# Optimization experiments

Measured on AMD Instinct MI355X. Metric: run time of the kernel, lower is better.

Reference implementation:

```python
import jax, jax.numpy as jnp
import numpy as np

H = 1024   # GRU hidden size
Z = 1024   # latent z dim
A = 4      # action dim
F = 30     # number of expert MLPs / max horizon
DIN = Z + H      # 2048, expert MLP input
DH = 512         # expert MLP hidden
EIN = H + 94     # evalMLP input (belief + pos/ori one-hot)
EH = 512
EOUT = 94


def setup_inputs() -> dict:
    key = jax.random.key(0)
    ks = jax.random.split(key, 20)
    s = 0.02
    inp = {
        "b_t": jax.random.normal(ks[0], (1, H), jnp.float32),
        "a_t": jax.random.normal(ks[1], (F, A), jnp.float32),
        "z_tp1_pos": jax.random.normal(ks[2], (F, Z), jnp.float32),
        "z_tp1_neg": jax.random.normal(ks[3], (F, Z), jnp.float32),
        "init_pos_ori": jax.random.uniform(ks[4], (1, 94), jnp.float32),
        # action GRU params (PyTorch layout: W_ih (3H, A), W_hh (3H, H))
        "gru_Wih": jax.random.normal(ks[5], (3 * H, A), jnp.float32) * s,
        "gru_Whh": jax.random.normal(ks[6], (3 * H, H), jnp.float32) * s,
        "gru_bih": jax.random.normal(ks[7], (3 * H,), jnp.float32) * s,
        "gru_bhh": jax.random.normal(ks[8], (3 * H,), jnp.float32) * s,
        # 30 stacked expert MLPs: Linear(DIN,DH)+ReLU+Linear(DH,1)
        "mlp_W1": jax.random.normal(ks[9], (F, DIN, DH), jnp.float32) * s,
        "mlp_b1": jax.random.normal(ks[10], (F, DH), jnp.float32) * s,
        "mlp_W2": jax.random.normal(ks[11], (F, DH, 1), jnp.float32) * s,
        "mlp_b2": jax.random.normal(ks[12], (F, 1), jnp.float32) * s,
        # evalMLP: Linear(EIN,EH)+ReLU+Linear(EH,EOUT)+sigmoid
        "eval_W1": jax.random.normal(ks[13], (EIN, EH), jnp.float32) * s,
        "eval_b1": jax.random.normal(ks[14], (EH,), jnp.float32) * s,
        "eval_W2": jax.random.normal(ks[15], (EH, EOUT), jnp.float32) * s,
        "eval_b2": jax.random.normal(ks[16], (EOUT,), jnp.float32) * s,
        "f": F,
    }
    return inp


def _gru(x, h0, Wih, Whh, bih, bhh):
    # x: (T, A), h0: (H,) -> outputs (T, H). PyTorch nn.GRU cell math.
    def step(h, xt):
        gi = Wih @ xt + bih          # (3H,)
        gh = Whh @ h + bhh           # (3H,)
        ir, iz, inn = jnp.split(gi, 3)
        hr, hz, hn = jnp.split(gh, 3)
        r = jax.nn.sigmoid(ir + hr)
        z = jax.nn.sigmoid(iz + hz)
        n = jnp.tanh(inn + r * hn)
        h_new = (1.0 - z) * n + z * h
        return h_new, h_new
    _, hs = jax.lax.scan(step, h0, x)
    return hs


def _experts(x, W1, b1, W2, b2, f):
    # x: (f, DIN); expert i applied to row i only (grouped batch-1 GEMMs).
    h = jax.nn.relu(jnp.einsum('fi,fih->fh', x, W1[:f]) + b1[:f])
    return jnp.einsum('fh,fho->fo', h, W2[:f]) + b2[:f]   # (f, 1) logits


def reference(b_t, a_t, z_tp1_pos, z_tp1_neg, init_pos_ori,
              gru_Wih, gru_Whh, gru_bih, gru_bhh,
              mlp_W1, mlp_b1, mlp_W2, mlp_b2,
              eval_W1, eval_b1, eval_W2, eval_b2, f):
    a_gru = _gru(a_t[:f], b_t[0], gru_Wih, gru_Whh, gru_bih, gru_bhh)  # (f, H)
    z_pos = jnp.concatenate([z_tp1_pos[:f], a_gru], axis=1)           # (f, Z+H)
    pred_positive = _experts(z_pos, mlp_W1, mlp_b1, mlp_W2, mlp_b2, f)
    z_neg = jnp.concatenate([z_tp1_neg[:f], a_gru], axis=1)
    pred_negative = _experts(z_neg, mlp_W1, mlp_b1, mlp_W2, mlp_b2, f)
    # eval branch uses b_t.detach()
    eval_in = jnp.concatenate([jax.lax.stop_gradient(b_t), init_pos_ori], axis=1)
    eh = jax.nn.relu(eval_in @ eval_W1 + eval_b1)
    pred_xytheta = jax.nn.sigmoid(eh @ eval_W2 + eval_b2)             # (1, 94)
    return pred_positive, pred_negative, pred_xytheta
```

## Files before the change

kernel.cpp:

```cpp
#include <hip/hip_runtime.h>
#include <math.h>

constexpr int kH    = 1024;
constexpr int kZ    = 1024;
constexpr int kA    = 4;
constexpr int kF    = 30;
constexpr int kDIN  = 2048;
constexpr int kDH   = 512;
constexpr int kEIN  = 1118;
constexpr int kEH   = 512;
constexpr int kEOUT = 94;

constexpr int GRU_NB  = 64;
constexpr int EXP_PRT = 8;

constexpr size_t HACC_OFF = 0;
constexpr size_t EHA_OFF  = HACC_OFF + (size_t)kF * 2 * EXP_PRT * kDH;
constexpr size_t TAG_OFF  = EHA_OFF + (size_t)8 * kEH;

__device__ __forceinline__ float sigmoidf_(float x) { return 1.0f / (1.0f + __expf(-x)); }

__device__ __forceinline__ float wave_reduce(float v) {
#pragma unroll
  for (int off = 32; off > 0; off >>= 1) v += __shfl_down(v, off, 64);
  return v;
}

__device__ __forceinline__ unsigned long long tag_ld(const unsigned long long* p) {
  return __hip_atomic_load(p, __ATOMIC_RELAXED, __HIP_MEMORY_SCOPE_AGENT);
}

__device__ __forceinline__ void tag_pub(unsigned long long* p, unsigned long long v) {
  (void)__hip_atomic_exchange(p, v, __ATOMIC_RELAXED, __HIP_MEMORY_SCOPE_AGENT);
}

__global__ __launch_bounds__(512) void gru64(const float* __restrict__ Whh,
                                             const float* __restrict__ bhh,
                                             const float* __restrict__ Wih,
                                             const float* __restrict__ bih,
                                             const float* __restrict__ a_t,
                                             const float* __restrict__ b_t,
                                             unsigned long long* __restrict__ tagbuf,
                                             const int* __restrict__ fptr) {
  const int bid  = blockIdx.x;
  const int tid  = threadIdx.x;
  const int wave = tid >> 6;
  const int lane = tid & 63;
  const int f    = *fptr;

  const int jb = bid * 16;
  const int j0 = jb + wave;
  const int j1 = jb + wave + 8;

  __shared__ float gis[kF][16][3];
  __shared__ __align__(16) float hs[kH];

  const float4* W4 = (const float4*)Whh;
  float4 wr0[4], wz0[4], wn0[4], wr1[4], wz1[4], wn1[4];
#pragma unroll
  for (int i = 0; i < 4; i++) {
    wr0[i] = W4[(size_t)j0 * 256 + i * 64 + lane];
    wz0[i] = W4[(size_t)(j0 + kH) * 256 + i * 64 + lane];
    wn0[i] = W4[(size_t)(j0 + 2 * kH) * 256 + i * 64 + lane];
    wr1[i] = W4[(size_t)j1 * 256 + i * 64 + lane];
    wz1[i] = W4[(size_t)(j1 + kH) * 256 + i * 64 + lane];
    wn1[i] = W4[(size_t)(j1 + 2 * kH) * 256 + i * 64 + lane];
  }
  const float b0r = bhh[j0], b0z = bhh[j0 + kH], b0n = bhh[j0 + 2 * kH];
  const float b1r = bhh[j1], b1z = bhh[j1 + kH], b1n = bhh[j1 + 2 * kH];

  for (int idx = tid; idx < kF * 16 * 3; idx += 512) {
    int t = idx / 48;
    int rem = idx - t * 48;
    int w = rem / 3, g = rem - w * 3;
    int r = jb + w + g * kH;
    float acc = bih[r];
    const float* wih = Wih + (size_t)r * kA;
    const float* at  = a_t + (size_t)t * kA;
#pragma unroll
    for (int k = 0; k < kA; k++) acc += wih[k] * at[k];
    gis[t][w][g] = acc;
  }
  __syncthreads();

  const float4* hs4 = (const float4*)hs;
  for (int t = 0; t < f; t++) {
    if (t == 0) {
      hs[tid]       = b_t[tid];
      hs[tid + 512] = b_t[tid + 512];
    } else {
      const unsigned long long* tg = tagbuf + (size_t)(t - 1) * kH;
      const unsigned want = (unsigned)t;
      unsigned long long v0 = tag_ld(tg + tid);
      unsigned long long v1 = tag_ld(tg + tid + 512);
      while ((unsigned)(v0 >> 32) != want) v0 = tag_ld(tg + tid);
      while ((unsigned)(v1 >> 32) != want) v1 = tag_ld(tg + tid + 512);
      hs[tid]       = __uint_as_float((unsigned)v0);
      hs[tid + 512] = __uint_as_float((unsigned)v1);
    }
    __syncthreads();

    float a0r = 0.f, a0z = 0.f, a0n = 0.f, a1r = 0.f, a1z = 0.f, a1n = 0.f;
#pragma unroll
    for (int i = 0; i < 4; i++) {
      float4 h4 = hs4[i * 64 + lane];
      a0r += wr0[i].x * h4.x + wr0[i].y * h4.y + wr0[i].z * h4.z + wr0[i].w * h4.w;
      a0z += wz0[i].x * h4.x + wz0[i].y * h4.y + wz0[i].z * h4.z + wz0[i].w * h4.w;
      a0n += wn0[i].x * h4.x + wn0[i].y * h4.y + wn0[i].z * h4.z + wn0[i].w * h4.w;
      a1r += wr1[i].x * h4.x + wr1[i].y * h4.y + wr1[i].z * h4.z + wr1[i].w * h4.w;
      a1z += wz1[i].x * h4.x + wz1[i].y * h4.y + wz1[i].z * h4.z + wz1[i].w * h4.w;
      a1n += wn1[i].x * h4.x + wn1[i].y * h4.y + wn1[i].z * h4.z + wn1[i].w * h4.w;
    }
    a0r = wave_reduce(a0r); a0z = wave_reduce(a0z); a0n = wave_reduce(a0n);
    a1r = wave_reduce(a1r); a1z = wave_reduce(a1z); a1n = wave_reduce(a1n);

    if (lane == 0) {
      float rg = sigmoidf_(gis[t][wave][0] + a0r + b0r);
      float zg = sigmoidf_(gis[t][wave][1] + a0z + b0z);
      float ng = tanhf(gis[t][wave][2] + rg * (a0n + b0n));
      float h0 = (1.0f - zg) * ng + zg * hs[j0];
      rg = sigmoidf_(gis[t][wave + 8][0] + a1r + b1r);
      zg = sigmoidf_(gis[t][wave + 8][1] + a1z + b1z);
      ng = tanhf(gis[t][wave + 8][2] + rg * (a1n + b1n));
      float h1 = (1.0f - zg) * ng + zg * hs[j1];

      const unsigned long long tg = (unsigned long long)(unsigned)(t + 1) << 32;
      tag_pub(tagbuf + (size_t)t * kH + j0, tg | (unsigned long long)__float_as_uint(h0));
      tag_pub(tagbuf + (size_t)t * kH + j1, tg | (unsigned long long)__float_as_uint(h1));
    }
    __syncthreads();
  }
}

__global__ __launch_bounds__(512) void experts(const float* __restrict__ zpos,
                                               const float* __restrict__ zneg,
                                               const unsigned long long* __restrict__ tagbuf,
                                               const float* __restrict__ W1,
                                               const float* __restrict__ b_t,
                                               const float* __restrict__ ipo,
                                               const float* __restrict__ eW1,
                                               float* __restrict__ hacc,
                                               float* __restrict__ ehacc,
                                               const int* __restrict__ fptr) {
  const int bid = blockIdx.x;
  const int tid = threadIdx.x;
  const int f   = *fptr;

  if (bid < kF * EXP_PRT) {
    __shared__ float xs_p[256];
    __shared__ float xs_n[256];
    int e = bid >> 3, part = bid & 7;
    if (e >= f) return;

    if (part < 4) {
      int r0 = part * 256;
      if (tid < 256) {
        xs_p[tid] = zpos[(size_t)e * kZ + r0 + tid];
        xs_n[tid] = zneg[(size_t)e * kZ + r0 + tid];
      }
      __syncthreads();
      float ap = 0.f, an = 0.f;
      const float* w = W1 + ((size_t)e * kDIN + r0) * kDH + tid;
#pragma unroll 8
      for (int r = 0; r < 256; r++) {
        float wv = w[(size_t)r * kDH];
        ap += xs_p[r] * wv;
        an += xs_n[r] * wv;
      }
      hacc[(((size_t)e * 2 + 0) * EXP_PRT + part) * kDH + tid] = ap;
      hacc[(((size_t)e * 2 + 1) * EXP_PRT + part) * kDH + tid] = an;
    } else {
      int r0 = (part - 4) * 256;
      if (tid < 256)
        xs_p[tid] = __uint_as_float((unsigned)tagbuf[(size_t)e * kH + r0 + tid]);
      __syncthreads();
      float a = 0.f;
      const float* w = W1 + ((size_t)e * kDIN + kZ + r0) * kDH + tid;
#pragma unroll 8
      for (int r = 0; r < 256; r++) a += xs_p[r] * w[(size_t)r * kDH];
      hacc[(((size_t)e * 2 + 0) * EXP_PRT + part) * kDH + tid] = a;
      hacc[(((size_t)e * 2 + 1) * EXP_PRT + part) * kDH + tid] = a;
    }
  } else {
    __shared__ float evs[140];
    int part = bid - kF * EXP_PRT;
    int r0 = part * 140;
    int nr = min(140, kEIN - r0);
    if (tid < nr) {
      int r = r0 + tid;
      evs[tid] = (r < kH) ? b_t[r] : ipo[r - kH];
    }
    __syncthreads();
    float acc = 0.f;
    const float* w = eW1 + (size_t)r0 * kEH + tid;
    for (int r = 0; r < nr; r++) acc += evs[r] * w[(size_t)r * kEH];
    ehacc[(size_t)part * kEH + tid] = acc;
  }
}

__global__ __launch_bounds__(512) void stage2(const float* __restrict__ hacc,
                                              const float* __restrict__ ehacc,
                                              const float* __restrict__ b1,
                                              const float* __restrict__ W2,
                                              const float* __restrict__ b2,
                                              const float* __restrict__ eb1,
                                              const float* __restrict__ eW2,
                                              const float* __restrict__ eb2,
                                              float* __restrict__ out,
                                              const int* __restrict__ fptr) {
  int b = blockIdx.x;
  int tid = threadIdx.x;
  int f = *fptr;
  if (b < kF) {
    int i = b;
    if (i >= f) return;
    float sp = 0.f, sn = 0.f;
#pragma unroll
    for (int p = 0; p < EXP_PRT; p++) {
      sp += hacc[(((size_t)i * 2 + 0) * EXP_PRT + p) * kDH + tid];
      sn += hacc[(((size_t)i * 2 + 1) * EXP_PRT + p) * kDH + tid];
    }
    float bias = b1[(size_t)i * kDH + tid];
    float hp = fmaxf(sp + bias, 0.f);
    float hn = fmaxf(sn + bias, 0.f);
    float w = W2[(size_t)i * kDH + tid];
    float pp = wave_reduce(hp * w);
    float pn = wave_reduce(hn * w);
    __shared__ float redp[8];
    __shared__ float redn[8];
    int wave = tid >> 6, lane = tid & 63;
    if (lane == 0) { redp[wave] = pp; redn[wave] = pn; }
    __syncthreads();
    if (tid == 0) {
      float s0 = 0.f, s1 = 0.f;
#pragma unroll
      for (int k = 0; k < 8; k++) { s0 += redp[k]; s1 += redn[k]; }
      out[i] = s0 + b2[i];
      out[f + i] = s1 + b2[i];
    }
  } else {
    __shared__ float ehs[kEH];
    {
      float s = eb1[tid];
#pragma unroll
      for (int p = 0; p < 8; p++) s += ehacc[(size_t)p * kEH + tid];
      ehs[tid] = fmaxf(s, 0.f);
    }
    __syncthreads();
    if (tid < kEOUT) {
      float acc = eb2[tid];
      for (int h = 0; h < kEH; h++) acc += ehs[h] * eW2[(size_t)h * kEOUT + tid];
      out[2 * f + tid] = sigmoidf_(acc);
    }
  }
}

extern "C" void kernel_launch(void* const* d_in, const int* in_sizes, int n_in,
                              void* d_out, int out_size, void* d_ws, size_t ws_size,
                              hipStream_t stream) {
  const float* b_t  = (const float*)d_in[0];
  const float* a_t  = (const float*)d_in[1];
  const float* zpos = (const float*)d_in[2];
  const float* zneg = (const float*)d_in[3];
  const float* ipo  = (const float*)d_in[4];
  const float* gWih = (const float*)d_in[5];
  const float* gWhh = (const float*)d_in[6];
  const float* gbih = (const float*)d_in[7];
  const float* gbhh = (const float*)d_in[8];
  const float* mW1  = (const float*)d_in[9];
  const float* mb1  = (const float*)d_in[10];
  const float* mW2  = (const float*)d_in[11];
  const float* mb2  = (const float*)d_in[12];
  const float* eW1  = (const float*)d_in[13];
  const float* eb1  = (const float*)d_in[14];
  const float* eW2  = (const float*)d_in[15];
  const float* eb2  = (const float*)d_in[16];
  const int*   fptr = (const int*)d_in[17];

  float* ws     = (float*)d_ws;
  float* hacc   = ws + HACC_OFF;
  float* ehacc  = ws + EHA_OFF;
  unsigned long long* tagbuf = (unsigned long long*)(ws + TAG_OFF);
  float* out    = (float*)d_out;

  gru64<<<GRU_NB, 512, 0, stream>>>(gWhh, gbhh, gWih, gbih, a_t, b_t, tagbuf, fptr);

  experts<<<kF * EXP_PRT + 8, 512, 0, stream>>>(zpos, zneg, tagbuf, mW1, b_t, ipo, eW1,
                                                hacc, ehacc, fptr);

  stage2<<<kF + 1, 512, 0, stream>>>(hacc, ehacc, mb1, mW2, mb2, eb1, eW2, eb2, out, fptr);
}
```

Before: 351.6 us.

## Spread GRU over 128 blocks with one hidden row per wave and LDS weights

The persistent GRU kernel now uses 128 blocks of 8 rows each instead of 64 blocks of 16. Each wave computes one hidden unit, and the W_hh slices move from registers into LDS (96 KB per block). The tag publish changes from an atomic exchange to an atomic store. The aim is to halve per-wave work on the serial critical path and cut register pressure. In exchange, twice as many blocks poll the tag buffer each step, and every step reads the weights from LDS instead of registers.

Result: faster. 342.7 us (-2.5%).

```diff
diff --git a/kernel.cpp b/kernel.cpp
--- a/kernel.cpp
+++ b/kernel.cpp
@@ -11,7 +11,8 @@
 constexpr int kEH   = 512;
 constexpr int kEOUT = 94;
 
-constexpr int GRU_NB  = 64;
+constexpr int GRU_NB = 128;
+constexpr int RPB    = 8;
 constexpr int EXP_PRT = 8;
 
 constexpr size_t HACC_OFF = 0;
@@ -29,49 +30,43 @@
 __device__ __forceinline__ unsigned long long tag_ld(const unsigned long long* p) {
   return __hip_atomic_load(p, __ATOMIC_RELAXED, __HIP_MEMORY_SCOPE_AGENT);
 }
-
-__device__ __forceinline__ void tag_pub(unsigned long long* p, unsigned long long v) {
-  (void)__hip_atomic_exchange(p, v, __ATOMIC_RELAXED, __HIP_MEMORY_SCOPE_AGENT);
-}
-
-__global__ __launch_bounds__(512) void gru64(const float* __restrict__ Whh,
-                                             const float* __restrict__ bhh,
-                                             const float* __restrict__ Wih,
-                                             const float* __restrict__ bih,
-                                             const float* __restrict__ a_t,
-                                             const float* __restrict__ b_t,
-                                             unsigned long long* __restrict__ tagbuf,
-                                             const int* __restrict__ fptr) {
+__device__ __forceinline__ void tag_st(unsigned long long* p, unsigned long long v) {
+  __hip_atomic_store(p, v, __ATOMIC_RELAXED, __HIP_MEMORY_SCOPE_AGENT);
+}
+
+__global__ __launch_bounds__(512) void gru128(const float* __restrict__ Whh,
+                                              const float* __restrict__ bhh,
+                                              const float* __restrict__ Wih,
+                                              const float* __restrict__ bih,
+                                              const float* __restrict__ a_t,
+                                              const float* __restrict__ b_t,
+                                              unsigned long long* __restrict__ tagbuf,
+                                              const int* __restrict__ fptr) {
   const int bid  = blockIdx.x;
   const int tid  = threadIdx.x;
   const int wave = tid >> 6;
   const int lane = tid & 63;
   const int f    = *fptr;
 
-  const int jb = bid * 16;
-  const int j0 = jb + wave;
-  const int j1 = jb + wave + 8;
-
-  __shared__ float gis[kF][16][3];
+  const int jb = bid * RPB;
+  const int j  = jb + wave;
+
+  __shared__ float4 wlds[RPB * 3 * 256];
+  __shared__ float gis[kF][RPB][3];
   __shared__ __align__(16) float hs[kH];
 
   const float4* W4 = (const float4*)Whh;
-  float4 wr0[4], wz0[4], wn0[4], wr1[4], wz1[4], wn1[4];
-#pragma unroll
-  for (int i = 0; i < 4; i++) {
-    wr0[i] = W4[(size_t)j0 * 256 + i * 64 + lane];
-    wz0[i] = W4[(size_t)(j0 + kH) * 256 + i * 64 + lane];
-    wn0[i] = W4[(size_t)(j0 + 2 * kH) * 256 + i * 64 + lane];
-    wr1[i] = W4[(size_t)j1 * 256 + i * 64 + lane];
-    wz1[i] = W4[(size_t)(j1 + kH) * 256 + i * 64 + lane];
-    wn1[i] = W4[(size_t)(j1 + 2 * kH) * 256 + i * 64 + lane];
-  }
-  const float b0r = bhh[j0], b0z = bhh[j0 + kH], b0n = bhh[j0 + 2 * kH];
-  const float b1r = bhh[j1], b1z = bhh[j1 + kH], b1n = bhh[j1 + 2 * kH];
-
-  for (int idx = tid; idx < kF * 16 * 3; idx += 512) {
-    int t = idx / 48;
-    int rem = idx - t * 48;
+  for (int idx = tid; idx < RPB * 3 * 256; idx += 512) {
+    int r = idx / 768;
+    int rem = idx - r * 768;
+    int g = rem >> 8;
+    int i = rem & 255;
+    wlds[idx] = W4[(size_t)(jb + r + g * kH) * 256 + i];
+  }
+
+  for (int idx = tid; idx < kF * RPB * 3; idx += 512) {
+    int t = idx / 24;
+    int rem = idx - t * 24;
     int w = rem / 3, g = rem - w * 3;
     int r = jb + w + g * kH;
     float acc = bih[r];
@@ -83,7 +78,12 @@
   }
   __syncthreads();
 
+  const float4* wr = wlds + (wave * 3 + 0) * 256;
+  const float4* wz = wlds + (wave * 3 + 1) * 256;
+  const float4* wn = wlds + (wave * 3 + 2) * 256;
+  const float br = bhh[j], bz = bhh[j + kH], bn = bhh[j + 2 * kH];
   const float4* hs4 = (const float4*)hs;
+
   for (int t = 0; t < f; t++) {
     if (t == 0) {
       hs[tid]       = b_t[tid];
@@ -100,33 +100,29 @@
     }
     __syncthreads();
 
-    float a0r = 0.f, a0z = 0.f, a0n = 0.f, a1r = 0.f, a1z = 0.f, a1n = 0.f;
+    float ar = 0.f, az = 0.f, an = 0.f;
 #pragma unroll
     for (int i = 0; i < 4; i++) {
       float4 h4 = hs4[i * 64 + lane];
-      a0r += wr0[i].x * h4.x + wr0[i].y * h4.y + wr0[i].z * h4.z + wr0[i].w * h4.w;
-      a0z += wz0[i].x * h4.x + wz0[i].y * h4.y + wz0[i].z * h4.z + wz0[i].w * h4.w;
-      a0n += wn0[i].x * h4.x + wn0[i].y * h4.y + wn0[i].z * h4.z + wn0[i].w * h4.w;
-      a1r += wr1[i].x * h4.x + wr1[i].y * h4.y + wr1[i].z * h4.z + wr1[i].w * h4.w;
-      a1z += wz1[i].x * h4.x + wz1[i].y * h4.y + wz1[i].z * h4.z + wz1[i].w * h4.w;
-      a1n += wn1[i].x * h4.x + wn1[i].y * h4.y + wn1[i].z * h4.z + wn1[i].w * h4.w;
-    }
-    a0r = wave_reduce(a0r); a0z = wave_reduce(a0z); a0n = wave_reduce(a0n);
-    a1r = wave_reduce(a1r); a1z = wave_reduce(a1z); a1n = wave_reduce(a1n);
+      float4 a = wr[i * 64 + lane];
+      float4 b = wz[i * 64 + lane];
+      float4 c = wn[i * 64 + lane];
+      ar += a.x * h4.x + a.y * h4.y + a.z * h4.z + a.w * h4.w;
+      az += b.x * h4.x + b.y * h4.y + b.z * h4.z + b.w * h4.w;
+      an += c.x * h4.x + c.y * h4.y + c.z * h4.z + c.w * h4.w;
+    }
+    ar = wave_reduce(ar);
+    az = wave_reduce(az);
+    an = wave_reduce(an);
 
     if (lane == 0) {
-      float rg = sigmoidf_(gis[t][wave][0] + a0r + b0r);
-      float zg = sigmoidf_(gis[t][wave][1] + a0z + b0z);
-      float ng = tanhf(gis[t][wave][2] + rg * (a0n + b0n));
-      float h0 = (1.0f - zg) * ng + zg * hs[j0];
-      rg = sigmoidf_(gis[t][wave + 8][0] + a1r + b1r);
-      zg = sigmoidf_(gis[t][wave + 8][1] + a1z + b1z);
-      ng = tanhf(gis[t][wave + 8][2] + rg * (a1n + b1n));
-      float h1 = (1.0f - zg) * ng + zg * hs[j1];
-
-      const unsigned long long tg = (unsigned long long)(unsigned)(t + 1) << 32;
-      tag_pub(tagbuf + (size_t)t * kH + j0, tg | (unsigned long long)__float_as_uint(h0));
-      tag_pub(tagbuf + (size_t)t * kH + j1, tg | (unsigned long long)__float_as_uint(h1));
+      float rg = sigmoidf_(gis[t][wave][0] + ar + br);
+      float zg = sigmoidf_(gis[t][wave][1] + az + bz);
+      float ng = tanhf(gis[t][wave][2] + rg * (an + bn));
+      float hn = (1.0f - zg) * ng + zg * hs[j];
+      tag_st(tagbuf + (size_t)t * kH + j,
+             ((unsigned long long)(unsigned)(t + 1) << 32) |
+                 (unsigned long long)__float_as_uint(hn));
     }
     __syncthreads();
   }
@@ -283,7 +279,7 @@
   unsigned long long* tagbuf = (unsigned long long*)(ws + TAG_OFF);
   float* out    = (float*)d_out;
 
-  gru64<<<GRU_NB, 512, 0, stream>>>(gWhh, gbhh, gWih, gbih, a_t, b_t, tagbuf, fptr);
+  gru128<<<GRU_NB, 512, 0, stream>>>(gWhh, gbhh, gWih, gbih, a_t, b_t, tagbuf, fptr);
 
   experts<<<kF * EXP_PRT + 8, 512, 0, stream>>>(zpos, zneg, tagbuf, mW1, b_t, ipo, eW1,
                                                 hacc, ehacc, fptr);
```
